# Optimization experiments

Hardware: AMD Instinct MI355X
Metric: run time of the kernel (lower is better)

Reference implementation:

```python
import jax, jax.numpy as jnp
import numpy as np

B, C, C1, C2, H, W = 16, 64, 16, 64, 128, 128

def setup_inputs() -> dict:
    key = jax.random.key(0)
    ks = jax.random.split(key, 8)
    s1 = 1.0 / np.sqrt(C1)
    s2 = 1.0 / np.sqrt(C)
    return {
        "x": jax.random.normal(ks[0], (B, C, H, W), dtype=jnp.float32),
        "e": jax.random.normal(ks[1], (B, C1, H, W), dtype=jnp.float32),
        "W1": jax.random.uniform(ks[2], (C2, C1), jnp.float32, -s1, s1),
        "b1": jax.random.uniform(ks[3], (C2,), jnp.float32, -s1, s1),
        "W2": jax.random.uniform(ks[4], (C2, C), jnp.float32, -s2, s2),
        "b2": jax.random.uniform(ks[5], (C2,), jnp.float32, -s2, s2),
        "W3": jax.random.uniform(ks[6], (C2, C), jnp.float32, -s2, s2),
        "b3": jax.random.uniform(ks[7], (C2,), jnp.float32, -s2, s2),
    }

def _conv1x1(inp, Wm, bv):
    # (B,Cin,H,W) x (Cout,Cin) -> (B,Cout,H,W)
    return jnp.einsum('bchw,oc->bohw', inp, Wm) + bv[None, :, None, None]

def reference(x, e, W1, b1, W2, b2, W3, b3):
    Bn, _, Hn, Wn = x.shape
    Q = _conv1x1(e, W1, b1).reshape(-1, Hn, Wn)   # (B*C2, H, W)
    V = _conv1x1(x, W2, b2).reshape(-1, Hn, Wn)
    K = _conv1x1(x, W3, b3).reshape(-1, Hn, Wn)
    score = jnp.einsum('nhw,ngw->nhg', Q, V)      # (B*C2, H, H), no scaling
    attn = jax.nn.softmax(score, axis=-1)
    ctx = jnp.einsum('nhg,ngw->nhw', attn, K)     # (B*C2, H, W)
    return ctx.reshape(Bn, -1, Hn, Wn)
```

## Files before the change

### kernel.cpp

```cpp
#include <hip/hip_runtime.h>

typedef __bf16 bf16_t;
typedef __bf16 bf16x8 __attribute__((ext_vector_type(8)));
typedef float f32x4 __attribute__((ext_vector_type(4)));
typedef unsigned short u16x4_t __attribute__((ext_vector_type(4)));

#define HW 16384
#define LOG2E 1.44269504088896f

__device__ __forceinline__ bf16_t f2b(float f) {
  unsigned u = __builtin_bit_cast(unsigned, f);
  u += 0x7fff + ((u >> 16) & 1);
  unsigned short s = (unsigned short)(u >> 16);
  return __builtin_bit_cast(bf16_t, s);
}
__device__ __forceinline__ unsigned short b2u(bf16_t b) {
  return __builtin_bit_cast(unsigned short, b);
}
__device__ __forceinline__ int swz8(int row) { return ((row ^ (row >> 3)) & 7) << 4; }
__device__ __forceinline__ int swz4v(int row) { return (row ^ (row >> 2)) & 3; }

__global__ __launch_bounds__(256, 3) void qvk_kernel(
    const float* __restrict__ x, const float* __restrict__ e,
    const float* __restrict__ W1, const float* __restrict__ b1,
    const float* __restrict__ W2, const float* __restrict__ b2,
    const float* __restrict__ W3, const float* __restrict__ b3,
    bf16_t* __restrict__ Qg, bf16_t* __restrict__ Vg, bf16_t* __restrict__ Kg)
{
  __shared__ bf16_t lx[128 * 64];
  __shared__ bf16_t le[128 * 32];
  __shared__ bf16_t w2b[64 * 64];
  __shared__ bf16_t w3b[64 * 64];
  __shared__ bf16_t w1b[64 * 32];
  __shared__ bf16_t rep[32 * 128];

  const int t = threadIdx.x;
  const int lane = t & 63;
  const int wv = t >> 6;
  const int b = blockIdx.x >> 7;
  const int p0 = (blockIdx.x & 127) << 7;
  const int lr = lane & 15;
  const int lg = lane >> 4;
  const int kq = lg << 3;

  const int li = lane & 31;
  const int h2 = lane >> 5;
  const int cbase = wv * 16 + h2 * 8;
  f32x4 xr[8];
#pragma unroll
  for (int j = 0; j < 8; ++j)
    xr[j] = *reinterpret_cast<const f32x4*>(
        x + (size_t)(b * 64 + cbase + j) * HW + p0 + li * 4);

  const int ec = t >> 4;
  const int ep = (t & 15) * 4;
  f32x4 er[2];
#pragma unroll
  for (int j = 0; j < 2; ++j)
    er[j] = *reinterpret_cast<const f32x4*>(
        e + (size_t)(b * 16 + ec) * HW + p0 + ep + j * 64);

  const int wo = t >> 2;
  const int wc = (t & 3) * 16;
  f32x4 w2r[4], w3r[4];
#pragma unroll
  for (int k = 0; k < 4; ++k) {
    w2r[k] = *reinterpret_cast<const f32x4*>(W2 + (size_t)wo * 64 + wc + k * 4);
    w3r[k] = *reinterpret_cast<const f32x4*>(W3 + (size_t)wo * 64 + wc + k * 4);
  }
  const int w1c = (t & 3) * 4;
  f32x4 w1r = *reinterpret_cast<const f32x4*>(W1 + (size_t)wo * 16 + w1c);

  float bv1[4], bv2[4], bv3[4];
#pragma unroll
  for (int nt = 0; nt < 4; ++nt) {
    bv1[nt] = b1[nt * 16 + lr];
    bv2[nt] = b2[nt * 16 + lr];
    bv3[nt] = b3[nt * 16 + lr];
  }

  {
    const int chunk = cbase >> 3;
#pragma unroll
    for (int r = 0; r < 4; ++r) {
      const int row = li * 4 + r;
      bf16x8 v;
#pragma unroll
      for (int j = 0; j < 8; ++j) v[j] = f2b(xr[j][r]);
      *reinterpret_cast<bf16x8*>(reinterpret_cast<char*>(lx)
          + row * 128 + ((chunk << 4) ^ swz8(row))) = v;
    }
  }
#pragma unroll
  for (int j = 0; j < 2; ++j)
#pragma unroll
    for (int r = 0; r < 4; ++r) {
      const int row = ep + j * 64 + r;
      const int byte = row * 64 + ((((ec >> 3) ^ swz4v(row)) << 4)) + (ec & 7) * 2;
      *reinterpret_cast<bf16_t*>(reinterpret_cast<char*>(le) + byte) = f2b(er[j][r]);
    }
  {
    const int row = t >> 1;
    const int chunk = 2 + (t & 1);
    bf16x8 zv;
#pragma unroll
    for (int k = 0; k < 8; ++k) zv[k] = f2b(0.0f);
    *reinterpret_cast<bf16x8*>(reinterpret_cast<char*>(le)
        + row * 64 + ((chunk ^ swz4v(row)) << 4)) = zv;
  }
  {
    const int ch0 = (t & 3) * 2;
    bf16x8 a, c2;
#pragma unroll
    for (int k = 0; k < 8; ++k) {
      a[k]  = f2b(w2r[k >> 2][k & 3]);
      c2[k] = f2b(w2r[2 + (k >> 2)][k & 3]);
    }
    *reinterpret_cast<bf16x8*>(reinterpret_cast<char*>(w2b)
        + wo * 128 + ((ch0 << 4) ^ swz8(wo))) = a;
    *reinterpret_cast<bf16x8*>(reinterpret_cast<char*>(w2b)
        + wo * 128 + (((ch0 + 1) << 4) ^ swz8(wo))) = c2;
#pragma unroll
    for (int k = 0; k < 8; ++k) {
      a[k]  = f2b(w3r[k >> 2][k & 3]);
      c2[k] = f2b(w3r[2 + (k >> 2)][k & 3]);
    }
    *reinterpret_cast<bf16x8*>(reinterpret_cast<char*>(w3b)
        + wo * 128 + ((ch0 << 4) ^ swz8(wo))) = a;
    *reinterpret_cast<bf16x8*>(reinterpret_cast<char*>(w3b)
        + wo * 128 + (((ch0 + 1) << 4) ^ swz8(wo))) = c2;
  }
  {
    typedef __bf16 bf16x4_ __attribute__((ext_vector_type(4)));
    bf16x4_ a;
#pragma unroll
    for (int k = 0; k < 4; ++k) a[k] = f2b(w1r[k]);
    const int byte = wo * 64 + (((w1c >> 3) ^ swz4v(wo)) << 4) + (w1c & 4) * 2;
    *reinterpret_cast<bf16x4_*>(reinterpret_cast<char*>(w1b) + byte) = a;
    if (t < 128) {
      const int row = t >> 1;
      const int chunk = 2 + (t & 1);
      bf16x8 zv;
#pragma unroll
      for (int k = 0; k < 8; ++k) zv[k] = f2b(0.0f);
      *reinterpret_cast<bf16x8*>(reinterpret_cast<char*>(w1b)
          + row * 64 + ((chunk ^ swz4v(row)) << 4)) = zv;
    }
  }
  __syncthreads();

  const int pw0 = wv << 5;

  auto ldx = [&](int row, int ce) -> bf16x8 {
    return *reinterpret_cast<const bf16x8*>(reinterpret_cast<const char*>(lx)
        + row * 128 + (((ce >> 3) << 4) ^ swz8(row)));
  };
  auto ldw = [&](const bf16_t* wb, int row, int ce) -> bf16x8 {
    return *reinterpret_cast<const bf16x8*>(reinterpret_cast<const char*>(wb)
        + row * 128 + (((ce >> 3) << 4) ^ swz8(row)));
  };
  auto ld64 = [&](const bf16_t* buf, int row, int ce) -> bf16x8 {
    return *reinterpret_cast<const bf16x8*>(reinterpret_cast<const char*>(buf)
        + row * 64 + (((ce >> 3) ^ swz4v(row)) << 4));
  };

  f32x4 acc[2][4];

  auto store_repack = [&](const float* bvv, bf16_t* __restrict__ G) {
#pragma unroll
    for (int half = 0; half < 2; ++half) {
#pragma unroll
      for (int q = 0; q < 2; ++q) {
        const int nt = half * 2 + q;
        const int ro = q * 16 + lr;
#pragma unroll
        for (int mt = 0; mt < 2; ++mt) {
          u16x4_t pk;
#pragma unroll
          for (int r = 0; r < 4; ++r) pk[r] = b2u(f2b(acc[mt][nt][r] + bvv[nt]));
          const int byte = ro * 256 + ((((pw0 + mt * 16 + (lg << 2)) << 1)) ^ swz8(ro));
          *reinterpret_cast<u16x4_t*>(reinterpret_cast<char*>(rep) + byte) = pk;
        }
      }
      __syncthreads();
      {
        const int ro = t >> 3;
        const int cb = (t & 7) * 32;
        bf16x8 v0 = *reinterpret_cast<const bf16x8*>(
            reinterpret_cast<const char*>(rep) + ro * 256 + (cb ^ swz8(ro)));
        bf16x8 v1 = *reinterpret_cast<const bf16x8*>(
            reinterpret_cast<const char*>(rep) + ro * 256 + ((cb + 16) ^ swz8(ro)));
        bf16_t* gp = G + (size_t)(b * 64 + half * 32 + ro) * HW + p0 + (t & 7) * 16;
        *reinterpret_cast<bf16x8*>(gp) = v0;
        *reinterpret_cast<bf16x8*>(gp + 8) = v1;
      }
      __syncthreads();
    }
  };

  auto do_xtarget = [&](const bf16_t* wb, const float* bvv, bf16_t* __restrict__ G) {
#pragma unroll
    for (int mt = 0; mt < 2; ++mt)
#pragma unroll
      for (int nt = 0; nt < 4; ++nt) acc[mt][nt] = f32x4{0.f, 0.f, 0.f, 0.f};
#pragma unroll
    for (int kt = 0; kt < 2; ++kt) {
      bf16x8 Af[2], Bw[4];
#pragma unroll
      for (int mt = 0; mt < 2; ++mt) Af[mt] = ldx(pw0 + mt * 16 + lr, kt * 32 + kq);
#pragma unroll
      for (int nt = 0; nt < 4; ++nt) Bw[nt] = ldw(wb, nt * 16 + lr, kt * 32 + kq);
#pragma unroll
      for (int mt = 0; mt < 2; ++mt)
#pragma unroll
        for (int nt = 0; nt < 4; ++nt)
          acc[mt][nt] = __builtin_amdgcn_mfma_f32_16x16x32_bf16(Af[mt], Bw[nt], acc[mt][nt], 0, 0, 0);
    }
    store_repack(bvv, G);
  };

  do_xtarget(w2b, bv2, Vg);
  do_xtarget(w3b, bv3, Kg);

#pragma unroll
  for (int mt = 0; mt < 2; ++mt)
#pragma unroll
    for (int nt = 0; nt < 4; ++nt) acc[mt][nt] = f32x4{0.f, 0.f, 0.f, 0.f};
  {
    bf16x8 Af[2], Bw[4];
#pragma unroll
    for (int mt = 0; mt < 2; ++mt) Af[mt] = ld64(le, pw0 + mt * 16 + lr, kq);
#pragma unroll
    for (int nt = 0; nt < 4; ++nt) Bw[nt] = ld64(w1b, nt * 16 + lr, kq);
#pragma unroll
    for (int mt = 0; mt < 2; ++mt)
#pragma unroll
      for (int nt = 0; nt < 4; ++nt)
        acc[mt][nt] = __builtin_amdgcn_mfma_f32_16x16x32_bf16(Af[mt], Bw[nt], acc[mt][nt], 0, 0, 0);
  }
  store_repack(bv1, Qg);
}

__global__ __launch_bounds__(512, 2) void attn_kernel(
    const bf16_t* __restrict__ Qg, const bf16_t* __restrict__ Vg,
    const bf16_t* __restrict__ Kg, float* __restrict__ out)
{
  __shared__ bf16_t bufK[128 * 128];
  __shared__ bf16_t bufV[128 * 128];
  __shared__ float zl[128];

  const int n = blockIdx.x;
  const int t = threadIdx.x;
  const int lane = t & 63;
  const int wv = t >> 6;
  const int lr = lane & 15;
  const int lg = lane >> 4;
  const int kq = lg << 3;
  const int h0 = wv << 4;

  const bf16_t* Qn = Qg + (size_t)n * HW;
  const bf16_t* Vn = Vg + (size_t)n * HW;
  const bf16_t* Kn = Kg + (size_t)n * HW;

  bf16x8 vreg[4];
#pragma unroll
  for (int it = 0; it < 4; ++it)
    vreg[it] = *reinterpret_cast<const bf16x8*>(Vn + (it * 512 + t) * 8);

  const int wchunk = t & 15;
  const int grow = t >> 4;
  bf16x8 kreg[4];
#pragma unroll
  for (int it = 0; it < 4; ++it)
    kreg[it] = *reinterpret_cast<const bf16x8*>(Kn + (grow + 32 * it) * 128 + wchunk * 8);

  bf16x8 qf[4];
#pragma unroll
  for (int kt = 0; kt < 4; ++kt)
    qf[kt] = *reinterpret_cast<const bf16x8*>(Qn + (h0 + lr) * 128 + kt * 32 + kq);

#pragma unroll
  for (int it = 0; it < 4; ++it) {
    const int chunk = it * 512 + t;
    const int row = chunk >> 4;
    *reinterpret_cast<bf16x8*>(reinterpret_cast<char*>(bufV)
        + row * 256 + (((chunk & 15) << 4) ^ swz8(row))) = vreg[it];
  }
  __syncthreads();

  auto ldfrag = [&](const bf16_t* buf, int row, int c) -> bf16x8 {
    return *reinterpret_cast<const bf16x8*>(reinterpret_cast<const char*>(buf)
        + row * 256 + (((c << 1)) ^ swz8(row)));
  };

  f32x4 acc[8];
#pragma unroll
  for (int nt = 0; nt < 8; ++nt) acc[nt] = f32x4{0.f, 0.f, 0.f, 0.f};
#pragma unroll
  for (int kt = 0; kt < 4; ++kt) {
#pragma unroll
    for (int nt = 0; nt < 8; ++nt) {
      bf16x8 Bv = ldfrag(bufV, nt * 16 + lr, kt * 32 + kq);
      acc[nt] = __builtin_amdgcn_mfma_f32_16x16x32_bf16(qf[kt], Bv, acc[nt], 0, 0, 0);
    }
  }

#pragma unroll
  for (int it = 0; it < 4; ++it) {
    const int g = grow + 32 * it;
#pragma unroll
    for (int j = 0; j < 8; ++j) {
      const int w = wchunk * 8 + j;
      *reinterpret_cast<bf16_t*>(reinterpret_cast<char*>(bufK)
          + w * 256 + ((g << 1) ^ swz8(w))) = kreg[it][j];
    }
  }

  float zrow[4];
#pragma unroll
  for (int r = 0; r < 4; ++r) {
    float m = acc[0][r];
#pragma unroll
    for (int nt = 1; nt < 8; ++nt) m = fmaxf(m, acc[nt][r]);
    m = fmaxf(m, __shfl_xor(m, 1));
    m = fmaxf(m, __shfl_xor(m, 2));
    m = fmaxf(m, __shfl_xor(m, 4));
    m = fmaxf(m, __shfl_xor(m, 8));
    float z = 0.f;
#pragma unroll
    for (int nt = 0; nt < 8; ++nt) {
      float p = exp2f((acc[nt][r] - m) * LOG2E);
      acc[nt][r] = p;
      z += p;
    }
    z += __shfl_xor(z, 1);
    z += __shfl_xor(z, 2);
    z += __shfl_xor(z, 4);
    z += __shfl_xor(z, 8);
    zrow[r] = z;
  }
  __syncthreads();

  {
    const int rbase = h0 + (lg << 2);
    if (lr == 0) {
#pragma unroll
      for (int r = 0; r < 4; ++r) zl[rbase + r] = 1.0f / zrow[r];
    }
#pragma unroll
    for (int nt = 0; nt < 8; ++nt) {
#pragma unroll
      for (int r = 0; r < 4; ++r) {
        const int row = rbase + r;
        *reinterpret_cast<bf16_t*>(reinterpret_cast<char*>(bufV)
            + row * 256 + (((nt * 16 + lr) << 1) ^ swz8(row))) = f2b(acc[nt][r]);
      }
    }
  }
  __syncthreads();

  f32x4 acc2[8];
#pragma unroll
  for (int nt = 0; nt < 8; ++nt) acc2[nt] = f32x4{0.f, 0.f, 0.f, 0.f};
#pragma unroll
  for (int kt = 0; kt < 4; ++kt) {
    bf16x8 A0 = ldfrag(bufK, h0 + lr, kt * 32 + kq);
#pragma unroll
    for (int nt = 0; nt < 8; ++nt) {
      bf16x8 Bp = ldfrag(bufV, nt * 16 + lr, kt * 32 + kq);
      acc2[nt] = __builtin_amdgcn_mfma_f32_16x16x32_bf16(A0, Bp, acc2[nt], 0, 0, 0);
    }
  }

  float* On = out + (size_t)n * HW;
#pragma unroll
  for (int nt = 0; nt < 8; ++nt) {
    const float zv = zl[nt * 16 + lr];
    f32x4 o;
#pragma unroll
    for (int r = 0; r < 4; ++r) o[r] = acc2[nt][r] * zv;
    *reinterpret_cast<f32x4*>(On + (size_t)(nt * 16 + lr) * 128
                              + h0 + (lg << 2)) = o;
  }
}

extern "C" void kernel_launch(void* const* d_in, const int* in_sizes, int n_in,
                              void* d_out, int out_size, void* d_ws, size_t ws_size,
                              hipStream_t stream) {
  const float* x  = (const float*)d_in[0];
  const float* e  = (const float*)d_in[1];
  const float* W1 = (const float*)d_in[2];
  const float* b1 = (const float*)d_in[3];
  const float* W2 = (const float*)d_in[4];
  const float* b2 = (const float*)d_in[5];
  const float* W3 = (const float*)d_in[6];
  const float* b3 = (const float*)d_in[7];
  float* out = (float*)d_out;

  bf16_t* Qg = (bf16_t*)d_ws;
  bf16_t* Vg = Qg + (size_t)1024 * HW;
  bf16_t* Kg = Vg + (size_t)1024 * HW;

  qvk_kernel<<<2048, 256, 0, stream>>>(x, e, W1, b1, W2, b2, W3, b3, Qg, Vg, Kg);
  attn_kernel<<<1024, 512, 0, stream>>>(Qg, Vg, Kg, out);
}
```

Before: 203.2 us.

## Load conv weights directly into MFMA fragments and drop LDS repack stores

The projection kernel no longer stages W1/W2/W3 in shared memory. Each lane loads its bf16 B-fragment straight from global fp32 weights. The outputs are written directly from accumulators as 8-byte stores instead of being repacked through LDS with extra barriers. This cuts LDS footprint and syncs, and occupancy hints are raised for both kernels. The cost is narrower, less coalesced global stores and redundant weight loads per wave, and the attn_kernel bound change may force register spills.

```diff
diff --git a/kernel.cpp b/kernel.cpp
--- a/kernel.cpp
+++ b/kernel.cpp
@@ -20,7 +20,7 @@
 __device__ __forceinline__ int swz8(int row) { return ((row ^ (row >> 3)) & 7) << 4; }
 __device__ __forceinline__ int swz4v(int row) { return (row ^ (row >> 2)) & 3; }
 
-__global__ __launch_bounds__(256, 3) void qvk_kernel(
+__global__ __launch_bounds__(256, 4) void qvk_kernel(
     const float* __restrict__ x, const float* __restrict__ e,
     const float* __restrict__ W1, const float* __restrict__ b1,
     const float* __restrict__ W2, const float* __restrict__ b2,
@@ -29,10 +29,6 @@
 {
   __shared__ bf16_t lx[128 * 64];
   __shared__ bf16_t le[128 * 32];
-  __shared__ bf16_t w2b[64 * 64];
-  __shared__ bf16_t w3b[64 * 64];
-  __shared__ bf16_t w1b[64 * 32];
-  __shared__ bf16_t rep[32 * 128];
 
   const int t = threadIdx.x;
   const int lane = t & 63;
@@ -60,17 +56,6 @@
     er[j] = *reinterpret_cast<const f32x4*>(
         e + (size_t)(b * 16 + ec) * HW + p0 + ep + j * 64);
 
-  const int wo = t >> 2;
-  const int wc = (t & 3) * 16;
-  f32x4 w2r[4], w3r[4];
-#pragma unroll
-  for (int k = 0; k < 4; ++k) {
-    w2r[k] = *reinterpret_cast<const f32x4*>(W2 + (size_t)wo * 64 + wc + k * 4);
-    w3r[k] = *reinterpret_cast<const f32x4*>(W3 + (size_t)wo * 64 + wc + k * 4);
-  }
-  const int w1c = (t & 3) * 4;
-  f32x4 w1r = *reinterpret_cast<const f32x4*>(W1 + (size_t)wo * 16 + w1c);
-
   float bv1[4], bv2[4], bv3[4];
 #pragma unroll
   for (int nt = 0; nt < 4; ++nt) {
@@ -108,45 +93,6 @@
     *reinterpret_cast<bf16x8*>(reinterpret_cast<char*>(le)
         + row * 64 + ((chunk ^ swz4v(row)) << 4)) = zv;
   }
-  {
-    const int ch0 = (t & 3) * 2;
-    bf16x8 a, c2;
-#pragma unroll
-    for (int k = 0; k < 8; ++k) {
-      a[k]  = f2b(w2r[k >> 2][k & 3]);
-      c2[k] = f2b(w2r[2 + (k >> 2)][k & 3]);
-    }
-    *reinterpret_cast<bf16x8*>(reinterpret_cast<char*>(w2b)
-        + wo * 128 + ((ch0 << 4) ^ swz8(wo))) = a;
-    *reinterpret_cast<bf16x8*>(reinterpret_cast<char*>(w2b)
-        + wo * 128 + (((ch0 + 1) << 4) ^ swz8(wo))) = c2;
-#pragma unroll
-    for (int k = 0; k < 8; ++k) {
-      a[k]  = f2b(w3r[k >> 2][k & 3]);
-      c2[k] = f2b(w3r[2 + (k >> 2)][k & 3]);
-    }
-    *reinterpret_cast<bf16x8*>(reinterpret_cast<char*>(w3b)
-        + wo * 128 + ((ch0 << 4) ^ swz8(wo))) = a;
-    *reinterpret_cast<bf16x8*>(reinterpret_cast<char*>(w3b)
-        + wo * 128 + (((ch0 + 1) << 4) ^ swz8(wo))) = c2;
-  }
-  {
-    typedef __bf16 bf16x4_ __attribute__((ext_vector_type(4)));
-    bf16x4_ a;
-#pragma unroll
-    for (int k = 0; k < 4; ++k) a[k] = f2b(w1r[k]);
-    const int byte = wo * 64 + (((w1c >> 3) ^ swz4v(wo)) << 4) + (w1c & 4) * 2;
-    *reinterpret_cast<bf16x4_*>(reinterpret_cast<char*>(w1b) + byte) = a;
-    if (t < 128) {
-      const int row = t >> 1;
-      const int chunk = 2 + (t & 1);
-      bf16x8 zv;
-#pragma unroll
-      for (int k = 0; k < 8; ++k) zv[k] = f2b(0.0f);
-      *reinterpret_cast<bf16x8*>(reinterpret_cast<char*>(w1b)
-          + row * 64 + ((chunk ^ swz4v(row)) << 4)) = zv;
-    }
-  }
   __syncthreads();
 
   const int pw0 = wv << 5;
@@ -155,72 +101,58 @@
     return *reinterpret_cast<const bf16x8*>(reinterpret_cast<const char*>(lx)
         + row * 128 + (((ce >> 3) << 4) ^ swz8(row)));
   };
-  auto ldw = [&](const bf16_t* wb, int row, int ce) -> bf16x8 {
-    return *reinterpret_cast<const bf16x8*>(reinterpret_cast<const char*>(wb)
-        + row * 128 + (((ce >> 3) << 4) ^ swz8(row)));
-  };
   auto ld64 = [&](const bf16_t* buf, int row, int ce) -> bf16x8 {
     return *reinterpret_cast<const bf16x8*>(reinterpret_cast<const char*>(buf)
         + row * 64 + (((ce >> 3) ^ swz4v(row)) << 4));
   };
+  auto wfrag = [&](const float* __restrict__ Wm, int nt, int kt) -> bf16x8 {
+    const float* wp = Wm + (size_t)(nt * 16 + lr) * 64 + kt * 32 + kq;
+    f32x4 a = *reinterpret_cast<const f32x4*>(wp);
+    f32x4 c = *reinterpret_cast<const f32x4*>(wp + 4);
+    bf16x8 v;
+#pragma unroll
+    for (int i = 0; i < 4; ++i) { v[i] = f2b(a[i]); v[4 + i] = f2b(c[i]); }
+    return v;
+  };
 
   f32x4 acc[2][4];
 
-  auto store_repack = [&](const float* bvv, bf16_t* __restrict__ G) {
-#pragma unroll
-    for (int half = 0; half < 2; ++half) {
-#pragma unroll
-      for (int q = 0; q < 2; ++q) {
-        const int nt = half * 2 + q;
-        const int ro = q * 16 + lr;
-#pragma unroll
-        for (int mt = 0; mt < 2; ++mt) {
-          u16x4_t pk;
-#pragma unroll
-          for (int r = 0; r < 4; ++r) pk[r] = b2u(f2b(acc[mt][nt][r] + bvv[nt]));
-          const int byte = ro * 256 + ((((pw0 + mt * 16 + (lg << 2)) << 1)) ^ swz8(ro));
-          *reinterpret_cast<u16x4_t*>(reinterpret_cast<char*>(rep) + byte) = pk;
-        }
+  auto do_xtarget = [&](const float* __restrict__ Wm, const float* bvv,
+                        bf16_t* __restrict__ G) {
+#pragma unroll
+    for (int mt = 0; mt < 2; ++mt)
+#pragma unroll
+      for (int nt = 0; nt < 4; ++nt) acc[mt][nt] = f32x4{0.f, 0.f, 0.f, 0.f};
+    bf16x8 Bw[2][4];
+#pragma unroll
+    for (int kt = 0; kt < 2; ++kt)
+#pragma unroll
+      for (int nt = 0; nt < 4; ++nt) Bw[kt][nt] = wfrag(Wm, nt, kt);
+#pragma unroll
+    for (int kt = 0; kt < 2; ++kt) {
+      bf16x8 Af[2];
+#pragma unroll
+      for (int mt = 0; mt < 2; ++mt) Af[mt] = ldx(pw0 + mt * 16 + lr, kt * 32 + kq);
+#pragma unroll
+      for (int mt = 0; mt < 2; ++mt)
+#pragma unroll
+        for (int nt = 0; nt < 4; ++nt)
+          acc[mt][nt] = __builtin_amdgcn_mfma_f32_16x16x32_bf16(Af[mt], Bw[kt][nt], acc[mt][nt], 0, 0, 0);
+    }
+#pragma unroll
+    for (int nt = 0; nt < 4; ++nt)
+#pragma unroll
+      for (int mt = 0; mt < 2; ++mt) {
+        u16x4_t pk;
+#pragma unroll
+        for (int r = 0; r < 4; ++r) pk[r] = b2u(f2b(acc[mt][nt][r] + bvv[nt]));
+        *reinterpret_cast<u16x4_t*>(G + (size_t)(b * 64 + nt * 16 + lr) * HW
+                                      + p0 + pw0 + mt * 16 + (lg << 2)) = pk;
       }
-      __syncthreads();
-      {
-        const int ro = t >> 3;
-        const int cb = (t & 7) * 32;
-        bf16x8 v0 = *reinterpret_cast<const bf16x8*>(
-            reinterpret_cast<const char*>(rep) + ro * 256 + (cb ^ swz8(ro)));
-        bf16x8 v1 = *reinterpret_cast<const bf16x8*>(
-            reinterpret_cast<const char*>(rep) + ro * 256 + ((cb + 16) ^ swz8(ro)));
-        bf16_t* gp = G + (size_t)(b * 64 + half * 32 + ro) * HW + p0 + (t & 7) * 16;
-        *reinterpret_cast<bf16x8*>(gp) = v0;
-        *reinterpret_cast<bf16x8*>(gp + 8) = v1;
-      }
-      __syncthreads();
-    }
-  };
-
-  auto do_xtarget = [&](const bf16_t* wb, const float* bvv, bf16_t* __restrict__ G) {
-#pragma unroll
-    for (int mt = 0; mt < 2; ++mt)
-#pragma unroll
-      for (int nt = 0; nt < 4; ++nt) acc[mt][nt] = f32x4{0.f, 0.f, 0.f, 0.f};
-#pragma unroll
-    for (int kt = 0; kt < 2; ++kt) {
-      bf16x8 Af[2], Bw[4];
-#pragma unroll
-      for (int mt = 0; mt < 2; ++mt) Af[mt] = ldx(pw0 + mt * 16 + lr, kt * 32 + kq);
-#pragma unroll
-      for (int nt = 0; nt < 4; ++nt) Bw[nt] = ldw(wb, nt * 16 + lr, kt * 32 + kq);
-#pragma unroll
-      for (int mt = 0; mt < 2; ++mt)
-#pragma unroll
-        for (int nt = 0; nt < 4; ++nt)
-          acc[mt][nt] = __builtin_amdgcn_mfma_f32_16x16x32_bf16(Af[mt], Bw[nt], acc[mt][nt], 0, 0, 0);
-    }
-    store_repack(bvv, G);
-  };
-
-  do_xtarget(w2b, bv2, Vg);
-  do_xtarget(w3b, bv3, Kg);
+  };
+
+  do_xtarget(W2, bv2, Vg);
+  do_xtarget(W3, bv3, Kg);
 
 #pragma unroll
   for (int mt = 0; mt < 2; ++mt)
@@ -229,19 +161,41 @@
   {
     bf16x8 Af[2], Bw[4];
 #pragma unroll
+    for (int nt = 0; nt < 4; ++nt) {
+      bf16x8 a;
+      if (kq < 16) {
+        const float* wp = W1 + (size_t)(nt * 16 + lr) * 16 + kq;
+        f32x4 lo = *reinterpret_cast<const f32x4*>(wp);
+        f32x4 hi = *reinterpret_cast<const f32x4*>(wp + 4);
+#pragma unroll
+        for (int i = 0; i < 4; ++i) { a[i] = f2b(lo[i]); a[4 + i] = f2b(hi[i]); }
+      } else {
+#pragma unroll
+        for (int i = 0; i < 8; ++i) a[i] = f2b(0.0f);
+      }
+      Bw[nt] = a;
+    }
+#pragma unroll
     for (int mt = 0; mt < 2; ++mt) Af[mt] = ld64(le, pw0 + mt * 16 + lr, kq);
-#pragma unroll
-    for (int nt = 0; nt < 4; ++nt) Bw[nt] = ld64(w1b, nt * 16 + lr, kq);
 #pragma unroll
     for (int mt = 0; mt < 2; ++mt)
 #pragma unroll
       for (int nt = 0; nt < 4; ++nt)
         acc[mt][nt] = __builtin_amdgcn_mfma_f32_16x16x32_bf16(Af[mt], Bw[nt], acc[mt][nt], 0, 0, 0);
   }
-  store_repack(bv1, Qg);
-}
-
-__global__ __launch_bounds__(512, 2) void attn_kernel(
+#pragma unroll
+  for (int nt = 0; nt < 4; ++nt)
+#pragma unroll
+    for (int mt = 0; mt < 2; ++mt) {
+      u16x4_t pk;
+#pragma unroll
+      for (int r = 0; r < 4; ++r) pk[r] = b2u(f2b(acc[mt][nt][r] + bv1[nt]));
+      *reinterpret_cast<u16x4_t*>(Qg + (size_t)(b * 64 + nt * 16 + lr) * HW
+                                    + p0 + pw0 + mt * 16 + (lg << 2)) = pk;
+    }
+}
+
+__global__ __launch_bounds__(512, 4) void attn_kernel(
     const bf16_t* __restrict__ Qg, const bf16_t* __restrict__ Vg,
     const bf16_t* __restrict__ Kg, float* __restrict__ out)
 {
```

After: 222.5 us. 1.09x slower.
